# Performance work log

Hardware: AMD Instinct MI355X
Metric: run time of the kernel (lower is better)

## Reference

```python
import jax, jax.numpy as jnp
import numpy as np

B = 64
SEQ = 192
LABEL = 48
PRED = 168
DEC_LEN = LABEL + PRED  # 216
ENC_IN = 7
DEC_IN = 7
C_OUT = 7
MARK = 4
D_MODEL = 1024
E_LAYERS = 2
D_LAYERS = 2


def setup_inputs() -> dict:
    key = jax.random.key(0)
    keys = iter(jax.random.split(key, 64))
    s = 1.0 / np.sqrt(D_MODEL)

    def u(shape):
        return jax.random.uniform(next(keys), shape, jnp.float32, -s, s)

    inp = {
        "x_enc": jax.random.normal(next(keys), (B, SEQ, ENC_IN), jnp.float32),
        "x_mark_enc": jax.random.normal(next(keys), (B, SEQ, MARK), jnp.float32),
        "x_dec": jax.random.normal(next(keys), (B, DEC_LEN, DEC_IN), jnp.float32),
        "x_mark_dec": jax.random.normal(next(keys), (B, DEC_LEN, MARK), jnp.float32),
    }
    for pfx, nl, in0 in (("enc", E_LAYERS, ENC_IN + MARK), ("dec", D_LAYERS, DEC_IN + MARK)):
        for l in range(nl):
            d_in = in0 if l == 0 else D_MODEL
            inp[f"{pfx}_W_ih_l{l}"] = u((3 * D_MODEL, d_in))
            inp[f"{pfx}_W_hh_l{l}"] = u((3 * D_MODEL, D_MODEL))
            inp[f"{pfx}_b_ih_l{l}"] = u((3 * D_MODEL,))
            inp[f"{pfx}_b_hh_l{l}"] = u((3 * D_MODEL,))
    inp["out_W"] = u((C_OUT, D_MODEL))
    inp["out_b"] = u((C_OUT,))
    return inp


def _gru_cell(x, h, W_ih, W_hh, b_ih, b_hh):
    # torch gate order: r, z, n
    gi = x @ W_ih.T + b_ih   # [B, 3H]
    gh = h @ W_hh.T + b_hh   # [B, 3H]
    i_r, i_z, i_n = jnp.split(gi, 3, axis=-1)
    h_r, h_z, h_n = jnp.split(gh, 3, axis=-1)
    r = jax.nn.sigmoid(i_r + h_r)
    z = jax.nn.sigmoid(i_z + h_z)
    n = jnp.tanh(i_n + r * h_n)
    return (1.0 - z) * n + z * h


def _stack_step(layers, h_layers, x_t):
    # layers: list of (W_ih, W_hh, b_ih, b_hh); h_layers: [L, B, H]
    inp = x_t
    new_h = []
    for l, (W_ih, W_hh, b_ih, b_hh) in enumerate(layers):
        hn = _gru_cell(inp, h_layers[l], W_ih, W_hh, b_ih, b_hh)
        new_h.append(hn)
        inp = hn
    return jnp.stack(new_h, axis=0), inp  # new hidden stack, top-layer output


def _forward(x_enc, x_mark_enc, x_dec, x_mark_dec, enc_layers, dec_layers, out_W, out_b):
    xe = jnp.concatenate([x_enc, x_mark_enc], axis=-1)  # [B, S, enc_in+4]
    xd = jnp.concatenate([x_dec, x_mark_dec], axis=-1)  # [B, T, dec_in+4]

    # --- encoder: multilayer GRU, keep only final hidden state ---
    h0 = jnp.zeros((E_LAYERS, B, D_MODEL), xe.dtype)

    def enc_step(h, x_t):
        h_new, _ = _stack_step(enc_layers, h, x_t)
        return h_new, None

    h_enc, _ = jax.lax.scan(enc_step, h0, jnp.swapaxes(xe, 0, 1))  # xs: [S, B, D]

    xd_t = jnp.swapaxes(xd, 0, 1)  # [T, B, dec_in+4]
    ts = jnp.arange(DEC_LEN)

    def dec_step(carry, xs):
        h, prev = carry
        x_t, t = xs
        marks = x_t[:, -MARK:]
        auto_in = jnp.concatenate([prev, marks], axis=-1)  # needs dec_in == c_out
        inp = jnp.where(t < LABEL, x_t, auto_in)
        h_new, out = _stack_step(dec_layers, h, inp)
        pred = out @ out_W.T + out_b  # [B, c_out]
        return (h_new, pred), pred

    prev0 = jnp.zeros((B, C_OUT), xd.dtype)
    _, preds = jax.lax.scan(dec_step, (h_enc, prev0), (xd_t, ts))  # [T, B, c_out]
    preds = jnp.swapaxes(preds, 0, 1)  # [B, T, c_out]
    return preds[:, -PRED:, :]


def reference(x_enc, x_mark_enc, x_dec, x_mark_dec,
              enc_W_ih_l0, enc_W_hh_l0, enc_b_ih_l0, enc_b_hh_l0,
              enc_W_ih_l1, enc_W_hh_l1, enc_b_ih_l1, enc_b_hh_l1,
              dec_W_ih_l0, dec_W_hh_l0, dec_b_ih_l0, dec_b_hh_l0,
              dec_W_ih_l1, dec_W_hh_l1, dec_b_ih_l1, dec_b_hh_l1,
              out_W, out_b):
    enc_layers = [
        (enc_W_ih_l0, enc_W_hh_l0, enc_b_ih_l0, enc_b_hh_l0),
        (enc_W_ih_l1, enc_W_hh_l1, enc_b_ih_l1, enc_b_hh_l1),
    ]
    dec_layers = [
        (dec_W_ih_l0, dec_W_hh_l0, dec_b_ih_l0, dec_b_hh_l0),
        (dec_W_ih_l1, dec_W_hh_l1, dec_b_ih_l1, dec_b_hh_l1),
    ]
    return _forward(x_enc, x_mark_enc, x_dec, x_mark_dec, enc_layers, dec_layers, out_W, out_b)
```

## Files before the change

kernel.cpp:

```cpp
#include <hip/hip_runtime.h>
#include <math.h>


typedef _Float16 half8 __attribute__((ext_vector_type(8)));
typedef _Float16 half4f __attribute__((ext_vector_type(4)));
typedef float f32x4 __attribute__((ext_vector_type(4)));

#define DM    1024
#define TENC  192
#define TDEC  216
#define LBL   48
#define NPRED 168
#define HB    131072
#define HE    65536

#define OFF_H0P0 8192
#define OFF_EH10 (OFF_H0P0 + 2*HB)
#define OFF_DH1  (OFF_EH10 + 2*HB)
#define OFF_WF   (OFF_DH1 + 217*HB)
#define OFF_BF0  (OFF_WF + 3072*1024*2)

#define L_TA0 0
#define L_TA1 32768
#define L_TB0 65536
#define L_TB1 98304
#define L_XW  131072
#define L_BA  131648
#define L_BAA 131712
#define L_BB  131776
#define L_TRA 131840
#define L_TRB 140032
#define L_HSTA 148224
#define L_HSTB 148736
#define SMEM_BYTES 149248

__device__ __forceinline__ float sigm(float x) { return 1.0f / (1.0f + __expf(-x)); }

__device__ __forceinline__ void coh_store64(void* p, unsigned long long v) {
  asm volatile("global_store_dwordx2 %0, %1, off sc0 sc1" :: "v"(p), "v"(v) : "memory");
}
__device__ __forceinline__ unsigned coh_load32(const void* p) {
  unsigned r;
  asm volatile("global_load_dword %0, %1, off sc0 sc1\n\ts_waitcnt vmcnt(0)"
               : "=v"(r) : "v"(p) : "memory");
  return r;
}
__device__ __forceinline__ half8 coh_load_h8(const void* p) {
  half8 r;
  asm volatile("global_load_dwordx4 %0, %1, off sc0 sc1" : "=v"(r) : "v"(p));
  return r;
}
__device__ __forceinline__ void ysync16(half8* y) {
  asm volatile("s_waitcnt vmcnt(0)"
               : "+v"(y[0]), "+v"(y[1]), "+v"(y[2]), "+v"(y[3]),
                 "+v"(y[4]), "+v"(y[5]), "+v"(y[6]), "+v"(y[7]),
                 "+v"(y[8]), "+v"(y[9]), "+v"(y[10]), "+v"(y[11]),
                 "+v"(y[12]), "+v"(y[13]), "+v"(y[14]), "+v"(y[15])
               :: "memory");
}
__device__ __forceinline__ void ytie16(half8* y) {
  asm volatile(""
               : "+v"(y[0]), "+v"(y[1]), "+v"(y[2]), "+v"(y[3]),
                 "+v"(y[4]), "+v"(y[5]), "+v"(y[6]), "+v"(y[7]),
                 "+v"(y[8]), "+v"(y[9]), "+v"(y[10]), "+v"(y[11]),
                 "+v"(y[12]), "+v"(y[13]), "+v"(y[14]), "+v"(y[15])
               ::);
}

__device__ __forceinline__ void bar_arrive(unsigned* leaf, int tid, int bx) {
  asm volatile("s_waitcnt vmcnt(0)" ::: "memory");
  __syncthreads();
  if (tid == 0)
    __hip_atomic_fetch_add(&leaf[(bx >> 3) << 5], 1u,
                           __ATOMIC_RELAXED, __HIP_MEMORY_SCOPE_AGENT);
}
__device__ __forceinline__ void wave_wait(unsigned* leaf, int lane, int kb0, unsigned ep) {
  const unsigned tgt = ep * 8u;
  const unsigned* p = &leaf[(unsigned)(kb0 + (lane & 15)) << 5];
  bool myok = false;
  for (;;) {
    if (!myok) myok = (coh_load32(p) >= tgt);
    if (__all((int)myok)) break;
    __builtin_amdgcn_s_sleep(2);
  }
}

__device__ __forceinline__ void fill_tile_f32(char* smem, int off, const float* __restrict__ src,
                                              int u0, int g0, int g1, int g2, int g3, int tid) {
  const int w = tid >> 6, lane = tid & 63;
  int gsel[4] = {g0, g1, g2, g3};
#pragma unroll
  for (int mm = 0; mm < 2; ++mm) {
    const int m = w + mm * 8;
    const int g = gsel[m >> 2];
    const long srow = (g < 0) ? -1 : (long)g * DM + u0 + (m & 3);
#pragma unroll
    for (int p = 0; p < 4; ++p) {
      const int k = p * 256 + lane * 4;
      half4f hv;
      if (srow >= 0) {
        float4 v = *(const float4*)(src + srow * DM + k);
        hv = (half4f){(_Float16)v.x, (_Float16)v.y, (_Float16)v.z, (_Float16)v.w};
      } else {
        hv = (half4f){(_Float16)0.f, (_Float16)0.f, (_Float16)0.f, (_Float16)0.f};
      }
      const int kb = k >> 5, q = (k >> 3) & 3;
      const int elem = (kb * 64 + q * 16 + m) * 8 + (k & 7);
      *(half4f*)(smem + off + elem * 2) = hv;
    }
  }
}

__device__ __forceinline__ void fill_tile_f16(char* smem, int off, const _Float16* __restrict__ src,
                                              int u0, int g0, int g1, int g2, int g3, int tid) {
  const int w = tid >> 6, lane = tid & 63;
  int gsel[4] = {g0, g1, g2, g3};
#pragma unroll
  for (int mm = 0; mm < 2; ++mm) {
    const int m = w + mm * 8;
    const int g = gsel[m >> 2];
    const long srow = (g < 0) ? -1 : (long)g * DM + u0 + (m & 3);
#pragma unroll
    for (int p = 0; p < 4; ++p) {
      const int k = p * 256 + lane * 4;
      half4f hv;
      if (srow >= 0) hv = *(const half4f*)(src + srow * DM + k);
      else hv = (half4f){(_Float16)0.f, (_Float16)0.f, (_Float16)0.f, (_Float16)0.f};
      const int kb = k >> 5, q = (k >> 3) & 3;
      const int elem = (kb * 64 + q * 16 + m) * 8 + (k & 7);
      *(half4f*)(smem + off + elem * 2) = hv;
    }
  }
}

__device__ __forceinline__ void fill_small(char* smem, int u0, int tid,
    const float* __restrict__ Wih0, const float* __restrict__ bihA, const float* __restrict__ bhhA,
    const float* __restrict__ bih1, const float* __restrict__ bhh1, const float* __restrict__ bf0) {
  if (tid < 132) {
    const int rr = tid / 11, c = tid - rr * 11;
    const int g = rr >> 2, ul = rr & 3;
    ((float*)(smem + L_XW))[(g * 4 + ul) * 12 + c] = Wih0[(g * DM + u0 + ul) * 11 + c];
  }
  if (tid < 4) {
    const int u = u0 + tid;
    float* bA = (float*)(smem + L_BA);
    bA[tid] = bihA[u] + bhhA[u];
    bA[4 + tid] = bihA[DM + u] + bhhA[DM + u];
    bA[8 + tid] = bhhA[2 * DM + u];
    bA[12 + tid] = bihA[2 * DM + u];
    float* bB = (float*)(smem + L_BB);
    bB[tid] = bih1[u] + bhh1[u];
    bB[4 + tid] = bih1[DM + u] + bhh1[DM + u];
    bB[8 + tid] = bhh1[2 * DM + u];
    bB[12 + tid] = bih1[2 * DM + u];
    if (bf0) {
      float* bAa = (float*)(smem + L_BAA);
      bAa[tid] = bf0[u] + bhhA[u];
      bAa[4 + tid] = bf0[DM + u] + bhhA[DM + u];
      bAa[8 + tid] = bhhA[2 * DM + u];
      bAa[12 + tid] = bf0[2 * DM + u];
    }
  }
}

#define MFMA16 __builtin_amdgcn_mfma_f32_16x16x32_f16
#define ZERO4 ((f32x4){0.f, 0.f, 0.f, 0.f})

__device__ __forceinline__ void yload(half8* y, const _Float16* src, int kb0, int lane, int bs) {
  const half8* B = (const half8*)src + ((lane >> 4) << 6) + bs + (lane & 15);
#pragma unroll
  for (int i = 0; i < 16; ++i)
    y[i] = coh_load_h8(B + ((size_t)(kb0 + i) << 8));
}

__device__ __forceinline__ f32x4 gemm_reg(const char* smem, int toff, int kb0, int lane,
                                          const half8* y, f32x4 seed) {
  const half8* T = (const half8*)(smem + toff);
  f32x4 aE = seed, aO = ZERO4;
#pragma unroll
  for (int i = 0; i < 16; i += 2) {
    aE = MFMA16(T[((kb0 + i) << 6) + lane], y[i], aE, 0, 0, 0);
    aO = MFMA16(T[((kb0 + i + 1) << 6) + lane], y[i + 1], aO, 0, 0, 0);
  }
  return aE + aO;
}

__device__ __forceinline__ void tr_store(char* smem, int trOff, int w, int lane, f32x4 acc) {
  float* tr = (float*)(smem + trOff) + (w << 8);
  const int quad = lane >> 4, col = lane & 15;
  tr[(quad * 4 + 0) * 16 + col] = acc[0];
  tr[(quad * 4 + 1) * 16 + col] = acc[1];
  tr[(quad * 4 + 2) * 16 + col] = acc[2];
  tr[(quad * 4 + 3) * 16 + col] = acc[3];
}

__device__ __forceinline__ void x_pre(const char* smem, int xmode,
    const float* __restrict__ xin, const float* __restrict__ xmk,
    int t, int seqT, int b, int ul, float& xr, float& xz, float& xn) {
  const float* xw = (const float*)(smem + L_XW);
  xr = 0.f; xz = 0.f; xn = 0.f;
  if (xmode == 1) {
    const float* xp = xin + (size_t)(b * seqT + t) * 7;
#pragma unroll
    for (int c = 0; c < 7; ++c) {
      float v = xp[c];
      xr = fmaf(xw[ul * 12 + c], v, xr);
      xz = fmaf(xw[(4 + ul) * 12 + c], v, xz);
      xn = fmaf(xw[(8 + ul) * 12 + c], v, xn);
    }
  }
  const float* mp = xmk + (size_t)(b * seqT + t) * 4;
#pragma unroll
  for (int m = 0; m < 4; ++m) {
    float v = mp[m];
    xr = fmaf(xw[ul * 12 + 7 + m], v, xr);
    xz = fmaf(xw[(4 + ul) * 12 + 7 + m], v, xz);
    xn = fmaf(xw[(8 + ul) * 12 + 7 + m], v, xn);
  }
}

__device__ __forceinline__ void epi(char* smem, int trOff, int stOff, int wb,
                                    int biasOff, float pxr, float pxz, float pxn,
                                    int tid, float& hprev) {
  const int lane = tid & 63, w = tid >> 6;
  const int bg = w - wb;
  const int col = lane & 15, ul = lane >> 4;
  const float* t0 = (const float*)(smem + trOff) + (bg << 8);
  const float* t1 = t0 + (4 << 8);
  const int b = (bg << 4) + col;
  float vr  = t0[ul * 16 + col]        + t1[ul * 16 + col];
  float vz  = t0[(4 + ul) * 16 + col]  + t1[(4 + ul) * 16 + col];
  float vnh = t0[(8 + ul) * 16 + col]  + t1[(8 + ul) * 16 + col];
  float vni = t0[(12 + ul) * 16 + col] + t1[(12 + ul) * 16 + col];
  const float* bias = (const float*)(smem + biasOff);
  float rg = sigm(vr + bias[ul] + pxr);
  float zg = sigm(vz + bias[4 + ul] + pxz);
  float ng = tanhf((vni + bias[12 + ul] + pxn) + rg * (vnh + bias[8 + ul]));
  float hn = ng + zg * (hprev - ng);
  hprev = hn;
  ((_Float16*)(smem + stOff))[b * 4 + ul] = (_Float16)hn;
}

__device__ __forceinline__ void st8(_Float16* dst, int u0, int i, const char* stage) {
  unsigned long long v = *(const unsigned long long*)(stage + i * 8);
  char* gp = (char*)dst + (((size_t)(u0 >> 3)) * 64 + i) * 16 + (size_t)(u0 & 7) * 2;
  coh_store64(gp, v);
}

__global__ __launch_bounds__(256) void prep_wf(const float* __restrict__ dWih0,
                                               const float* __restrict__ dbih0,
                                               const float* __restrict__ outW,
                                               const float* __restrict__ outb,
                                               char* __restrict__ ws) {
  const int j = blockIdx.x;
  _Float16* wf = (_Float16*)(ws + OFF_WF);
  float* bf0 = (float*)(ws + OFF_BF0);
  float wrow[7];
#pragma unroll
  for (int c = 0; c < 7; ++c) wrow[c] = dWih0[j * 11 + c];
#pragma unroll
  for (int p = 0; p < 4; ++p) {
    const int k = p * 256 + threadIdx.x;
    float acc = 0.f;
#pragma unroll
    for (int c = 0; c < 7; ++c) acc = fmaf(wrow[c], outW[c * DM + k], acc);
    wf[(size_t)j * DM + k] = (_Float16)acc;
  }
  if (threadIdx.x == 0) {
    float bb = dbih0[j];
#pragma unroll
    for (int c = 0; c < 7; ++c) bb = fmaf(wrow[c], outb[c], bb);
    bf0[j] = bb;
  }
}

__global__ __launch_bounds__(512) void gru_persist(
    const float* __restrict__ xe,  const float* __restrict__ xme,
    const float* __restrict__ xd,  const float* __restrict__ xmd,
    const float* __restrict__ eWih0, const float* __restrict__ eWhh0,
    const float* __restrict__ ebih0, const float* __restrict__ ebhh0,
    const float* __restrict__ eWih1, const float* __restrict__ eWhh1,
    const float* __restrict__ ebih1, const float* __restrict__ ebhh1,
    const float* __restrict__ dWih0, const float* __restrict__ dWhh0,
    const float* __restrict__ dbih0, const float* __restrict__ dbhh0,
    const float* __restrict__ dWih1, const float* __restrict__ dWhh1,
    const float* __restrict__ dbih1, const float* __restrict__ dbhh1,
    char* __restrict__ ws) {
  extern __shared__ char smem[];
  const int tid = threadIdx.x, bx = blockIdx.x;
  const int lane = tid & 63;
  const int w = tid >> 6;
  const int bg = w & 3, kslice = w >> 2;
  const int bs = bg << 4, kb0 = kslice << 4;
  const int u0 = bx << 2;
  const int bA = ((w & 3) << 4) + (lane & 15);
  const int ulA = lane >> 4;

  unsigned* leaf = (unsigned*)ws;
  _Float16* h0p[2] = {(_Float16*)(ws + OFF_H0P0), (_Float16*)(ws + OFF_H0P0 + HB)};
  _Float16* eh1[2] = {(_Float16*)(ws + OFF_EH10), (_Float16*)(ws + OFF_EH10 + HB)};
  _Float16* dh1 = (_Float16*)(ws + OFF_DH1);
  const _Float16* wf = (const _Float16*)(ws + OFF_WF);
  const float* bf0 = (const float*)(ws + OFF_BF0);

  half8 y0[16], y1[16];
  f32x4 carryI = ZERO4, carryA = ZERO4, carryB = ZERO4;
  float pxr = 0.f, pxz = 0.f, pxn = 0.f;
  float hA = 0.f, hB = 0.f;
  unsigned ep = 0;

  fill_tile_f32(smem, L_TA0, eWhh0, u0, 0, 1, 2, -1, tid);
  fill_tile_f32(smem, L_TB0, eWih1, u0, 0, 1, -1, 2, tid);
  fill_tile_f32(smem, L_TB1, eWhh1, u0, 0, 1, 2, -1, tid);
  fill_small(smem, u0, tid, eWih0, ebih0, ebhh0, ebih1, ebhh1, nullptr);
  __syncthreads();
  if (w < 4) x_pre(smem, 1, xe, xme, 0, TENC, bA, ulA, pxr, pxz, pxn);

  for (int t = 0; t < TENC; ++t) {
    wave_wait(leaf, lane, kb0, ep);
    yload(y0, h0p[t & 1], kb0, lane, bs);
    if (t >= 2) yload(y1, eh1[(t - 3) & 1], kb0, lane, bs);
    ysync16(y0);
    if (t >= 2) ytie16(y1);
    f32x4 aA = gemm_reg(smem, L_TA0, kb0, lane, y0, ZERO4);
    tr_store(smem, L_TRA, w, lane, aA);
    if (t >= 2) {
      f32x4 aB = gemm_reg(smem, L_TB1, kb0, lane, y1, carryI);
      tr_store(smem, L_TRB, w, lane, aB);
    }
    __syncthreads();
    if (w < 4) epi(smem, L_TRA, L_HSTA, 0, L_BA, pxr, pxz, pxn, tid, hA);
    else if (t >= 2) epi(smem, L_TRB, L_HSTB, 4, L_BB, 0.f, 0.f, 0.f, tid, hB);
    __syncthreads();
    if (tid < 64) st8(h0p[(t & 1) ^ 1], u0, tid, smem + L_HSTA);
    else if (t >= 2 && tid < 128) st8(eh1[t & 1], u0, tid - 64, smem + L_HSTB);
    bar_arrive(leaf, tid, bx); ++ep;
    carryI = gemm_reg(smem, L_TB0, kb0, lane, y0, ZERO4);
    if (w < 4 && t + 1 < TENC) x_pre(smem, 1, xe, xme, t + 1, TENC, bA, ulA, pxr, pxz, pxn);
  }
  {
    wave_wait(leaf, lane, kb0, ep);
    yload(y0, h0p[0], kb0, lane, bs);
    yload(y1, eh1[1], kb0, lane, bs);
    ysync16(y0);
    ytie16(y1);
    f32x4 aB = gemm_reg(smem, L_TB1, kb0, lane, y1, carryI);
    tr_store(smem, L_TRB, w, lane, aB);
    __syncthreads();
    if (w >= 4) epi(smem, L_TRB, L_HSTB, 4, L_BB, 0.f, 0.f, 0.f, tid, hB);
    __syncthreads();
    if (tid >= 64 && tid < 128) st8(eh1[0], u0, tid - 64, smem + L_HSTB);
    bar_arrive(leaf, tid, bx); ++ep;
    carryI = gemm_reg(smem, L_TB0, kb0, lane, y0, ZERO4);
  }
  {
    wave_wait(leaf, lane, kb0, ep);
    yload(y1, eh1[0], kb0, lane, bs);
    ysync16(y1);
    f32x4 aB = gemm_reg(smem, L_TB1, kb0, lane, y1, carryI);
    tr_store(smem, L_TRB, w, lane, aB);
    __syncthreads();
    if (w >= 4) epi(smem, L_TRB, L_HSTB, 4, L_BB, 0.f, 0.f, 0.f, tid, hB);
    __syncthreads();
    if (tid >= 64 && tid < 128) st8(dh1, u0, tid - 64, smem + L_HSTB);
    bar_arrive(leaf, tid, bx); ++ep;
    fill_tile_f32(smem, L_TA0, dWhh0, u0, 0, 1, 2, -1, tid);
    fill_tile_f16(smem, L_TA1, wf,    u0, 0, 1, -1, 2, tid);
    fill_tile_f32(smem, L_TB0, dWih1, u0, 0, 1, -1, 2, tid);
    fill_tile_f32(smem, L_TB1, dWhh1, u0, 0, 1, 2, -1, tid);
    fill_small(smem, u0, tid, dWih0, dbih0, dbhh0, dbih1, dbhh1, bf0);
    __syncthreads();
    if (w < 4) x_pre(smem, 1, xd, xmd, 0, TDEC, bA, ulA, pxr, pxz, pxn);
  }

  for (int d = 0; d < LBL; ++d) {
    wave_wait(leaf, lane, kb0, ep);
    yload(y0, h0p[d & 1], kb0, lane, bs);
    if (d >= 2) yload(y1, dh1 + (size_t)(d - 2) * HE, kb0, lane, bs);
    ysync16(y0);
    if (d >= 2) ytie16(y1);
    f32x4 aA = gemm_reg(smem, L_TA0, kb0, lane, y0, ZERO4);
    tr_store(smem, L_TRA, w, lane, aA);
    if (d >= 2) {
      f32x4 aB = gemm_reg(smem, L_TB1, kb0, lane, y1, carryI);
      tr_store(smem, L_TRB, w, lane, aB);
    }
    __syncthreads();
    if (w < 4) epi(smem, L_TRA, L_HSTA, 0, L_BA, pxr, pxz, pxn, tid, hA);
    else if (d >= 2) epi(smem, L_TRB, L_HSTB, 4, L_BB, 0.f, 0.f, 0.f, tid, hB);
    __syncthreads();
    if (tid < 64) st8(h0p[(d & 1) ^ 1], u0, tid, smem + L_HSTA);
    else if (d >= 2 && tid < 128) st8(dh1 + (size_t)(d - 1) * HE, u0, tid - 64, smem + L_HSTB);
    bar_arrive(leaf, tid, bx); ++ep;
    carryI = gemm_reg(smem, L_TB0, kb0, lane, y0, ZERO4);
    if (w < 4 && d + 1 < LBL) x_pre(smem, 1, xd, xmd, d + 1, TDEC, bA, ulA, pxr, pxz, pxn);
  }
  {
    wave_wait(leaf, lane, kb0, ep);
    yload(y0, h0p[0], kb0, lane, bs);
    yload(y1, dh1 + (size_t)46 * HE, kb0, lane, bs);
    ysync16(y0);
    ytie16(y1);
    f32x4 aB = gemm_reg(smem, L_TB1, kb0, lane, y1, carryI);
    tr_store(smem, L_TRB, w, lane, aB);
    __syncthreads();
    if (w >= 4) epi(smem, L_TRB, L_HSTB, 4, L_BB, 0.f, 0.f, 0.f, tid, hB);
    __syncthreads();
    if (tid >= 64 && tid < 128) st8(dh1 + (size_t)47 * HE, u0, tid - 64, smem + L_HSTB);
    bar_arrive(leaf, tid, bx); ++ep;
    carryI = gemm_reg(smem, L_TB0, kb0, lane, y0, ZERO4);
    carryA = gemm_reg(smem, L_TA0, kb0, lane, y0, ZERO4);
  }
  {
    wave_wait(leaf, lane, kb0, ep);
    yload(y1, dh1 + (size_t)47 * HE, kb0, lane, bs);
    ysync16(y1);
    f32x4 aB = gemm_reg(smem, L_TB1, kb0, lane, y1, carryI);
    tr_store(smem, L_TRB, w, lane, aB);
    __syncthreads();
    if (w >= 4) epi(smem, L_TRB, L_HSTB, 4, L_BB, 0.f, 0.f, 0.f, tid, hB);
    __syncthreads();
    if (tid >= 64 && tid < 128) st8(dh1 + (size_t)48 * HE, u0, tid - 64, smem + L_HSTB);
    bar_arrive(leaf, tid, bx); ++ep;
    if (w < 4) x_pre(smem, 2, nullptr, xmd, LBL, TDEC, bA, ulA, pxr, pxz, pxn);
  }

  for (int s = LBL; s < TDEC; ++s) {
    wave_wait(leaf, lane, kb0, ep);
    yload(y1, dh1 + (size_t)s * HE, kb0, lane, bs);
    ysync16(y1);
    f32x4 aA = gemm_reg(smem, L_TA1, kb0, lane, y1, carryA);
    tr_store(smem, L_TRA, w, lane, aA);
    __syncthreads();
    if (w < 4) epi(smem, L_TRA, L_HSTA, 0, L_BAA, pxr, pxz, pxn, tid, hA);
    __syncthreads();
    if (tid < 64) st8(h0p[(s & 1) ^ 1], u0, tid, smem + L_HSTA);
    bar_arrive(leaf, tid, bx); ++ep;
    carryB = gemm_reg(smem, L_TB1, kb0, lane, y1, ZERO4);
    wave_wait(leaf, lane, kb0, ep);
    yload(y0, h0p[(s & 1) ^ 1], kb0, lane, bs);
    ysync16(y0);
    f32x4 aB = gemm_reg(smem, L_TB0, kb0, lane, y0, carryB);
    tr_store(smem, L_TRB, w, lane, aB);
    __syncthreads();
    if (w >= 4) epi(smem, L_TRB, L_HSTB, 4, L_BB, 0.f, 0.f, 0.f, tid, hB);
    __syncthreads();
    if (tid >= 64 && tid < 128) st8(dh1 + (size_t)(s + 1) * HE, u0, tid - 64, smem + L_HSTB);
    bar_arrive(leaf, tid, bx); ++ep;
    carryA = gemm_reg(smem, L_TA0, kb0, lane, y0, ZERO4);
    if (w < 4 && s + 1 < TDEC) x_pre(smem, 2, nullptr, xmd, s + 1, TDEC, bA, ulA, pxr, pxz, pxn);
  }
}

__global__ __launch_bounds__(64) void proj_kernel(const char* __restrict__ ws,
                                                  const float* __restrict__ outW,
                                                  const float* __restrict__ outb,
                                                  float* __restrict__ out) {
  const int ti = blockIdx.x / 7, c = blockIdx.x % 7;
  const _Float16* h = (const _Float16*)(ws + OFF_DH1) + (size_t)(LBL + 1 + ti) * HE;
  const int b = threadIdx.x;
  const float* wrow = outW + c * DM;
  float acc = outb[c];
#pragma unroll 4
  for (int k8 = 0; k8 < 128; ++k8) {
    const half8 hv = *(const half8*)(h + ((size_t)k8 * 64 + b) * 8);
    const float* wp = wrow + k8 * 8;
#pragma unroll
    for (int j = 0; j < 8; ++j) acc = fmaf((float)hv[j], wp[j], acc);
  }
  out[(size_t)b * (NPRED * 7) + ti * 7 + c] = acc;
}

extern "C" void kernel_launch(void* const* d_in, const int* in_sizes, int n_in,
                              void* d_out, int out_size, void* d_ws, size_t ws_size,
                              hipStream_t stream) {
  (void)in_sizes; (void)n_in; (void)out_size; (void)ws_size;
  const float* xe    = (const float*)d_in[0];
  const float* xme   = (const float*)d_in[1];
  const float* xd    = (const float*)d_in[2];
  const float* xmd   = (const float*)d_in[3];
  const float* eWih0 = (const float*)d_in[4];
  const float* eWhh0 = (const float*)d_in[5];
  const float* ebih0 = (const float*)d_in[6];
  const float* ebhh0 = (const float*)d_in[7];
  const float* eWih1 = (const float*)d_in[8];
  const float* eWhh1 = (const float*)d_in[9];
  const float* ebih1 = (const float*)d_in[10];
  const float* ebhh1 = (const float*)d_in[11];
  const float* dWih0 = (const float*)d_in[12];
  const float* dWhh0 = (const float*)d_in[13];
  const float* dbih0 = (const float*)d_in[14];
  const float* dbhh0 = (const float*)d_in[15];
  const float* dWih1 = (const float*)d_in[16];
  const float* dWhh1 = (const float*)d_in[17];
  const float* dbih1 = (const float*)d_in[18];
  const float* dbhh1 = (const float*)d_in[19];
  const float* outW  = (const float*)d_in[20];
  const float* outb  = (const float*)d_in[21];
  char* ws = (char*)d_ws;

  hipFuncSetAttribute(reinterpret_cast<const void*>(gru_persist),
                      hipFuncAttributeMaxDynamicSharedMemorySize, SMEM_BYTES);

  hipMemsetAsync(ws, 0, OFF_H0P0 + HB, stream);
  hipMemsetAsync(ws + OFF_EH10, 0, 2 * HB, stream);

  prep_wf<<<3072, 256, 0, stream>>>(dWih0, dbih0, outW, outb, ws);
  gru_persist<<<256, 512, SMEM_BYTES, stream>>>(xe, xme, xd, xmd,
                                                eWih0, eWhh0, ebih0, ebhh0,
                                                eWih1, eWhh1, ebih1, ebhh1,
                                                dWih0, dWhh0, dbih0, dbhh0,
                                                dWih1, dWhh1, dbih1, dbhh1, ws);
  proj_kernel<<<NPRED * 7, 64, 0, stream>>>(ws, outW, outb, (float*)d_out);
}
```

Measured before the change: 2.841 ms.

## Overlap barrier polling with per-chunk hidden-state loads as leaf counters become ready

Replaces the wave-wide wait-then-load sequence with a loop that polls each of the 16 leaf counters and immediately issues the coherent loads for whichever K-chunks are already complete. This lets hidden-state fetches start while other producer groups are still arriving, hiding part of the load latency behind the barrier wait on the recurrent critical path. The cost is more control flow and ballots per iteration, and the conditional loads may compile to less efficient scattered code with extra register pressure. The s_sleep backoff is also removed.

```diff
diff --git a/kernel.cpp b/kernel.cpp
--- a/kernel.cpp
+++ b/kernel.cpp
@@ -74,14 +74,47 @@
     __hip_atomic_fetch_add(&leaf[(bx >> 3) << 5], 1u,
                            __ATOMIC_RELAXED, __HIP_MEMORY_SCOPE_AGENT);
 }
-__device__ __forceinline__ void wave_wait(unsigned* leaf, int lane, int kb0, unsigned ep) {
+
+__device__ __forceinline__ void wait_load1(unsigned* leaf, int kb0, int lane, unsigned ep,
+                                           half8* y, const _Float16* src, int bs) {
   const unsigned tgt = ep * 8u;
   const unsigned* p = &leaf[(unsigned)(kb0 + (lane & 15)) << 5];
-  bool myok = false;
+  const half8* B = (const half8*)src + ((lane >> 4) << 6) + bs + (lane & 15);
+  unsigned done = 0u, pend = 0u;
   for (;;) {
-    if (!myok) myok = (coh_load32(p) >= tgt);
-    if (__all((int)myok)) break;
-    __builtin_amdgcn_s_sleep(2);
+#pragma unroll
+    for (int i = 0; i < 16; ++i)
+      if (pend & (1u << i)) y[i] = coh_load_h8(B + ((size_t)(kb0 + i) << 8));
+    done |= pend;
+    if (done == 0xFFFFu) break;
+    bool mine = ((done >> (lane & 15)) & 1u) != 0u;
+    if (!mine) mine = (coh_load32(p) >= tgt);
+    const unsigned ready = (unsigned)__ballot((int)mine) & 0xFFFFu;
+    pend = ready & ~done;
+  }
+}
+
+__device__ __forceinline__ void wait_load2(unsigned* leaf, int kb0, int lane, unsigned ep,
+                                           half8* ya, const _Float16* srcA,
+                                           half8* yb, const _Float16* srcB, int bs) {
+  const unsigned tgt = ep * 8u;
+  const unsigned* p = &leaf[(unsigned)(kb0 + (lane & 15)) << 5];
+  const half8* BA = (const half8*)srcA + ((lane >> 4) << 6) + bs + (lane & 15);
+  const half8* BB = (const half8*)srcB + ((lane >> 4) << 6) + bs + (lane & 15);
+  unsigned done = 0u, pend = 0u;
+  for (;;) {
+#pragma unroll
+    for (int i = 0; i < 16; ++i)
+      if (pend & (1u << i)) {
+        ya[i] = coh_load_h8(BA + ((size_t)(kb0 + i) << 8));
+        yb[i] = coh_load_h8(BB + ((size_t)(kb0 + i) << 8));
+      }
+    done |= pend;
+    if (done == 0xFFFFu) break;
+    bool mine = ((done >> (lane & 15)) & 1u) != 0u;
+    if (!mine) mine = (coh_load32(p) >= tgt);
+    const unsigned ready = (unsigned)__ballot((int)mine) & 0xFFFFu;
+    pend = ready & ~done;
   }
 }
 
@@ -165,13 +198,6 @@
 
 #define MFMA16 __builtin_amdgcn_mfma_f32_16x16x32_f16
 #define ZERO4 ((f32x4){0.f, 0.f, 0.f, 0.f})
-
-__device__ __forceinline__ void yload(half8* y, const _Float16* src, int kb0, int lane, int bs) {
-  const half8* B = (const half8*)src + ((lane >> 4) << 6) + bs + (lane & 15);
-#pragma unroll
-  for (int i = 0; i < 16; ++i)
-    y[i] = coh_load_h8(B + ((size_t)(kb0 + i) << 8));
-}
 
 __device__ __forceinline__ f32x4 gemm_reg(const char* smem, int toff, int kb0, int lane,
                                           const half8* y, f32x4 seed) {
@@ -317,11 +343,14 @@
   if (w < 4) x_pre(smem, 1, xe, xme, 0, TENC, bA, ulA, pxr, pxz, pxn);
 
   for (int t = 0; t < TENC; ++t) {
-    wave_wait(leaf, lane, kb0, ep);
-    yload(y0, h0p[t & 1], kb0, lane, bs);
-    if (t >= 2) yload(y1, eh1[(t - 3) & 1], kb0, lane, bs);
-    ysync16(y0);
-    if (t >= 2) ytie16(y1);
+    if (t >= 2) {
+      wait_load2(leaf, kb0, lane, ep, y0, h0p[t & 1], y1, eh1[(t - 3) & 1], bs);
+      ysync16(y0);
+      ytie16(y1);
+    } else {
+      wait_load1(leaf, kb0, lane, ep, y0, h0p[t & 1], bs);
+      ysync16(y0);
+    }
     f32x4 aA = gemm_reg(smem, L_TA0, kb0, lane, y0, ZERO4);
     tr_store(smem, L_TRA, w, lane, aA);
     if (t >= 2) {
@@ -339,9 +368,7 @@
     if (w < 4 && t + 1 < TENC) x_pre(smem, 1, xe, xme, t + 1, TENC, bA, ulA, pxr, pxz, pxn);
   }
   {
-    wave_wait(leaf, lane, kb0, ep);
-    yload(y0, h0p[0], kb0, lane, bs);
-    yload(y1, eh1[1], kb0, lane, bs);
+    wait_load2(leaf, kb0, lane, ep, y0, h0p[0], y1, eh1[1], bs);
     ysync16(y0);
     ytie16(y1);
     f32x4 aB = gemm_reg(smem, L_TB1, kb0, lane, y1, carryI);
@@ -354,8 +381,7 @@
     carryI = gemm_reg(smem, L_TB0, kb0, lane, y0, ZERO4);
   }
   {
-    wave_wait(leaf, lane, kb0, ep);
-    yload(y1, eh1[0], kb0, lane, bs);
+    wait_load1(leaf, kb0, lane, ep, y1, eh1[0], bs);
     ysync16(y1);
     f32x4 aB = gemm_reg(smem, L_TB1, kb0, lane, y1, carryI);
     tr_store(smem, L_TRB, w, lane, aB);
@@ -374,11 +400,14 @@
   }
 
   for (int d = 0; d < LBL; ++d) {
-    wave_wait(leaf, lane, kb0, ep);
-    yload(y0, h0p[d & 1], kb0, lane, bs);
-    if (d >= 2) yload(y1, dh1 + (size_t)(d - 2) * HE, kb0, lane, bs);
-    ysync16(y0);
-    if (d >= 2) ytie16(y1);
+    if (d >= 2) {
+      wait_load2(leaf, kb0, lane, ep, y0, h0p[d & 1], y1, dh1 + (size_t)(d - 2) * HE, bs);
+      ysync16(y0);
+      ytie16(y1);
+    } else {
+      wait_load1(leaf, kb0, lane, ep, y0, h0p[d & 1], bs);
+      ysync16(y0);
+    }
     f32x4 aA = gemm_reg(smem, L_TA0, kb0, lane, y0, ZERO4);
     tr_store(smem, L_TRA, w, lane, aA);
     if (d >= 2) {
@@ -396,9 +425,7 @@
     if (w < 4 && d + 1 < LBL) x_pre(smem, 1, xd, xmd, d + 1, TDEC, bA, ulA, pxr, pxz, pxn);
   }
   {
-    wave_wait(leaf, lane, kb0, ep);
-    yload(y0, h0p[0], kb0, lane, bs);
-    yload(y1, dh1 + (size_t)46 * HE, kb0, lane, bs);
+    wait_load2(leaf, kb0, lane, ep, y0, h0p[0], y1, dh1 + (size_t)46 * HE, bs);
     ysync16(y0);
     ytie16(y1);
     f32x4 aB = gemm_reg(smem, L_TB1, kb0, lane, y1, carryI);
@@ -412,8 +439,7 @@
     carryA = gemm_reg(smem, L_TA0, kb0, lane, y0, ZERO4);
   }
   {
-    wave_wait(leaf, lane, kb0, ep);
-    yload(y1, dh1 + (size_t)47 * HE, kb0, lane, bs);
+    wait_load1(leaf, kb0, lane, ep, y1, dh1 + (size_t)47 * HE, bs);
     ysync16(y1);
     f32x4 aB = gemm_reg(smem, L_TB1, kb0, lane, y1, carryI);
     tr_store(smem, L_TRB, w, lane, aB);
@@ -426,8 +452,7 @@
   }
 
   for (int s = LBL; s < TDEC; ++s) {
-    wave_wait(leaf, lane, kb0, ep);
-    yload(y1, dh1 + (size_t)s * HE, kb0, lane, bs);
+    wait_load1(leaf, kb0, lane, ep, y1, dh1 + (size_t)s * HE, bs);
     ysync16(y1);
     f32x4 aA = gemm_reg(smem, L_TA1, kb0, lane, y1, carryA);
     tr_store(smem, L_TRA, w, lane, aA);
@@ -437,8 +462,7 @@
     if (tid < 64) st8(h0p[(s & 1) ^ 1], u0, tid, smem + L_HSTA);
     bar_arrive(leaf, tid, bx); ++ep;
     carryB = gemm_reg(smem, L_TB1, kb0, lane, y1, ZERO4);
-    wave_wait(leaf, lane, kb0, ep);
-    yload(y0, h0p[(s & 1) ^ 1], kb0, lane, bs);
+    wait_load1(leaf, kb0, lane, ep, y0, h0p[(s & 1) ^ 1], bs);
     ysync16(y0);
     f32x4 aB = gemm_reg(smem, L_TB0, kb0, lane, y0, carryB);
     tr_store(smem, L_TRB, w, lane, aB);
```

New measurement: 3.355 ms. 1.18x slower.
